# Kernel optimization log

Hardware: AMD Instinct MI355X
Metric: run time of the kernel (lower is better)

Reference implementation:

```python
import jax, jax.numpy as jnp
import numpy as np

NUM_HEADS = 16

def setup_inputs() -> dict:
    key = jax.random.key(0)
    k1, k2, k3 = jax.random.split(key, 3)
    B, S, D = 2, 2048, 1024
    return {
        "hidden_states": jax.random.normal(k1, (B, S, D), dtype=jnp.float32),
        "W_attn": jax.random.normal(k2, (D, 3 * D), dtype=jnp.float32) * 0.02,
        "b_attn": jnp.zeros((3 * D,), dtype=jnp.float32),
        "W_proj": jax.random.normal(k3, (D, D), dtype=jnp.float32) * 0.02,
        "b_proj": jnp.zeros((D,), dtype=jnp.float32),
    }

def reference(hidden_states, W_attn, b_attn, W_proj, b_proj):
    B, S, D = hidden_states.shape
    H = NUM_HEADS
    hd = D // H
    # qkv projection (Conv1D == addmm): [B,S,3D]
    qkv = hidden_states @ W_attn + b_attn
    q, k, v = jnp.split(qkv, 3, axis=-1)
    # split heads -> [B,H,S,hd]
    def split_heads(t):
        return t.reshape(B, S, H, hd).transpose(0, 2, 1, 3)
    q, k, v = split_heads(q), split_heads(k), split_heads(v)
    # scaled QK^T: [B,H,S,S]
    scores = jnp.einsum('bhqd,bhkd->bhqk', q, k) / jnp.asarray(hd ** 0.5, dtype=q.dtype)
    causal = jnp.tril(jnp.ones((S, S), dtype=bool))
    mask_value = jnp.finfo(scores.dtype).min
    scores = jnp.where(causal, scores, mask_value)
    probs = jax.nn.softmax(scores, axis=-1)  # attn_pdrop=0 -> no dropout
    out = jnp.einsum('bhqk,bhkd->bhqd', probs, v)
    # merge heads -> [B,S,D]
    out = out.transpose(0, 2, 1, 3).reshape(B, S, D)
    out = out @ W_proj + b_proj  # resid_pdrop=0 -> no dropout
    return out
```

## Files before the change

kernel.cpp:

```cpp
#include <hip/hip_runtime.h>
#include <math.h>

typedef __attribute__((ext_vector_type(8))) short bf16x8;
typedef __attribute__((ext_vector_type(4))) short bf16x4;
typedef __attribute__((ext_vector_type(4))) float f32x4;

#define MFMA16(a, b, c) __builtin_amdgcn_mfma_f32_16x16x32_bf16(a, b, c, 0, 0, 0)

#define GLOAD_LDS16(g, l)                                                        \
    __builtin_amdgcn_global_load_lds(                                            \
        (const __attribute__((address_space(1))) void*)(g),                      \
        (__attribute__((address_space(3))) void*)(l), 16, 0, 0)

__device__ __forceinline__ short f2bf(float f) {
    union { float f; unsigned u; } x; x.f = f;
    unsigned r = (x.u + 0x7fffu + ((x.u >> 16) & 1u)) >> 16;
    return (short)r;
}

__global__ __launch_bounds__(256) void convert_bf16_kernel(
    const float* __restrict__ in, short* __restrict__ out, int n4) {
    int i = blockIdx.x * 256 + threadIdx.x;
    if (i >= n4) return;
    float4 v = ((const float4*)in)[i];
    bf16x4 o;
    o[0] = f2bf(v.x); o[1] = f2bf(v.y); o[2] = f2bf(v.z); o[3] = f2bf(v.w);
    ((bf16x4*)out)[i] = o;
}

__global__ __launch_bounds__(256) void transpose_w2_kernel(
    const float* __restrict__ Wa, const float* __restrict__ Wp,
    short* __restrict__ WaT, short* __restrict__ WpT) {
    __shared__ float tile[32][33];
    const float* W; short* Wt; int N, xb;
    if (blockIdx.x < 96) { W = Wa; Wt = WaT; N = 3072; xb = blockIdx.x; }
    else                 { W = Wp; Wt = WpT; N = 1024; xb = blockIdx.x - 96; }
    const int K = 1024;
    int c = threadIdx.x & 31, r0 = threadIdx.x >> 5;
    int n0 = xb << 5, k0 = blockIdx.y << 5;
#pragma unroll
    for (int i = 0; i < 4; i++) {
        int r = r0 + i * 8;
        tile[r][c] = W[(long)(k0 + r) * N + n0 + c];
    }
    __syncthreads();
#pragma unroll
    for (int i = 0; i < 4; i++) {
        int r = r0 + i * 8;
        Wt[(long)(n0 + r) * K + k0 + c] = f2bf(tile[c][r]);
    }
}


#define SBAR() __builtin_amdgcn_s_barrier()
#define PRIO(x) __builtin_amdgcn_s_setprio(x)
#define VMW4 asm volatile("s_waitcnt vmcnt(4)" ::: "memory")
#define VMW2 asm volatile("s_waitcnt vmcnt(2)" ::: "memory")
#define VMW0 asm volatile("s_waitcnt vmcnt(0)" ::: "memory")
#define NOPS ((void)0)

#define LDA8(IDX) (*(const bf16x8*)&ls[(IDX)])
#define SA(q, k1v, nbv) GLOAD_LDS16(Ags + (size_t)(q) * 65536 + (k1v), &ls[(nbv) + (q) * 4096 + swd])
#define SB(q, k1v, nbv) GLOAD_LDS16(Bgs + (size_t)(q) * 65536 + (k1v), &ls[(nbv) + 32768 + (q) * 4096 + swd])

#define PHASE_MFMA(M0_, M1_, aa0, ba0, aa1, ba1)              \
    PRIO(1);                                                  \
    acc[M0_][0] = MFMA16(aa0, b00, acc[M0_][0]);              \
    acc[M0_][1] = MFMA16(aa0, b10, acc[M0_][1]);              \
    acc[M0_][2] = MFMA16(aa0, b20, acc[M0_][2]);              \
    acc[M0_][3] = MFMA16(aa0, b30, acc[M0_][3]);              \
    acc[M1_][0] = MFMA16(ba0, b00, acc[M1_][0]);              \
    acc[M1_][1] = MFMA16(ba0, b10, acc[M1_][1]);              \
    acc[M1_][2] = MFMA16(ba0, b20, acc[M1_][2]);              \
    acc[M1_][3] = MFMA16(ba0, b30, acc[M1_][3]);              \
    acc[M0_][0] = MFMA16(aa1, b01, acc[M0_][0]);              \
    acc[M0_][1] = MFMA16(aa1, b11, acc[M0_][1]);              \
    acc[M0_][2] = MFMA16(aa1, b21, acc[M0_][2]);              \
    acc[M0_][3] = MFMA16(aa1, b31, acc[M0_][3]);              \
    acc[M1_][0] = MFMA16(ba1, b01, acc[M1_][0]);              \
    acc[M1_][1] = MFMA16(ba1, b11, acc[M1_][1]);              \
    acc[M1_][2] = MFMA16(ba1, b21, acc[M1_][2]);              \
    acc[M1_][3] = MFMA16(ba1, b31, acc[M1_][3]);              \
    PRIO(0);

#define KTILE(T, STG, VMP2, VMTAIL) do {                                              \
    const int cb = ((T) & 1) << 14;                                                   \
    const int nb = cb ^ 16384;                                                        \
    const int k1 = ((T) + 1) << 6;                                                    \
    (void)nb; (void)k1;                                                               \
                                                                    \
    if (STG) { SB(0, k1, nb); SB(1, k1, nb); }                                        \
    const bf16x8 b00 = LDA8(cb + 32768 + bro + sw0);                                  \
    const bf16x8 b01 = LDA8(cb + 32768 + bro + sw1);                                  \
    const bf16x8 b10 = LDA8(cb + 32768 + bro + 1024 + sw0);                           \
    const bf16x8 b11 = LDA8(cb + 32768 + bro + 1024 + sw1);                           \
    const bf16x8 b20 = LDA8(cb + 32768 + bro + 2048 + sw0);                           \
    const bf16x8 b21 = LDA8(cb + 32768 + bro + 2048 + sw1);                           \
    const bf16x8 b30 = LDA8(cb + 32768 + bro + 3072 + sw0);                           \
    const bf16x8 b31 = LDA8(cb + 32768 + bro + 3072 + sw1);                           \
    {                                                                                 \
        bf16x8 x0 = LDA8(cb + aro + sw0), x1 = LDA8(cb + aro + sw1);                  \
        bf16x8 y0 = LDA8(cb + aro + 1024 + sw0), y1 = LDA8(cb + aro + 1024 + sw1);    \
        SBAR();                                                                       \
        PHASE_MFMA(0, 1, x0, y0, x1, y1)                                              \
        SBAR();                                                                       \
    }                                                                                 \
                                                                    \
    if (STG) { SB(2, k1, nb); SB(3, k1, nb); }                                        \
    {                                                                                 \
        bf16x8 x0 = LDA8(cb + aro + 2048 + sw0), x1 = LDA8(cb + aro + 2048 + sw1);    \
        bf16x8 y0 = LDA8(cb + aro + 3072 + sw0), y1 = LDA8(cb + aro + 3072 + sw1);    \
        SBAR();                                                                       \
        PHASE_MFMA(2, 3, x0, y0, x1, y1)                                              \
        SBAR();                                                                       \
    }                                                                                 \
                                                                    \
    VMP2;                                                                             \
    SBAR();                                                                           \
    if (STG) { SA(0, k1, nb); SA(2, k1, nb); }                                        \
    {                                                                                 \
        bf16x8 x0 = LDA8(cb + aro + 4096 + sw0), x1 = LDA8(cb + aro + 4096 + sw1);    \
        bf16x8 y0 = LDA8(cb + aro + 5120 + sw0), y1 = LDA8(cb + aro + 5120 + sw1);    \
        PHASE_MFMA(4, 5, x0, y0, x1, y1)                                              \
        SBAR();                                                                       \
    }                                                                                 \
                                                                    \
    if (STG) { SA(1, k1, nb); SA(3, k1, nb); }                                        \
    {                                                                                 \
        bf16x8 x0 = LDA8(cb + aro + 6144 + sw0), x1 = LDA8(cb + aro + 6144 + sw1);    \
        bf16x8 y0 = LDA8(cb + aro + 7168 + sw0), y1 = LDA8(cb + aro + 7168 + sw1);    \
        SBAR();                                                                       \
        PHASE_MFMA(6, 7, x0, y0, x1, y1)                                              \
        VMTAIL;                                                                       \
        SBAR();                                                                       \
    }                                                                                 \
} while (0)

__global__ __launch_bounds__(512, 2) void gemm_qkv_kernel(
    const short* __restrict__ A, const short* __restrict__ Bt,
    const float* __restrict__ bias,
    short* __restrict__ QK, short* __restrict__ VTb) {
    __shared__ __align__(16) short ls[65536];
    const int tid = threadIdx.x;
    const int lane = tid & 63, l15 = lane & 15, quad = lane >> 4;
    const int w = tid >> 6, wm = w >> 2, wn = w & 3;
    const int m0 = blockIdx.y * 256, n0 = blockIdx.x * 256;
    const int e = l15 & 7;
    const int sgr = (w << 3) + (lane >> 3);
    const int sgc = ((lane & 7) ^ (lane >> 3)) << 3;
    const int swd = w << 9;
    const short* Ags = A + (size_t)(m0 + sgr) * 1024 + sgc;
    const short* Bgs = Bt + (size_t)(n0 + sgr) * 1024 + sgc;
    const int aro = (wm * 128 + l15) << 6;
    const int bro = (wn * 64 + l15) << 6;
    const int sw0 = (quad ^ e) << 3;
    const int sw1 = ((4 + quad) ^ e) << 3;

    f32x4 acc[8][4];
#pragma unroll
    for (int i = 0; i < 8; i++)
#pragma unroll
        for (int j = 0; j < 4; j++) acc[i][j] = (f32x4){0.f, 0.f, 0.f, 0.f};

    SB(0, 0, 0); SB(1, 0, 0); SB(2, 0, 0); SB(3, 0, 0);
    SA(0, 0, 0); SA(2, 0, 0); SA(1, 0, 0); SA(3, 0, 0);
    VMW2;
    SBAR();

#pragma unroll 2
    for (int t = 0; t < 14; ++t) { KTILE(t, 1, VMW4, VMW2); }
    KTILE(14, 1, VMW4, VMW0);
    KTILE(15, 0, VMW0, NOPS);

    __syncthreads();

    if (n0 < 2048) {
        const float scale = (n0 < 1024) ? 0.18033688011112042f : 1.0f;
#pragma unroll
        for (int nt = 0; nt < 4; nt++) {
            const int nn = n0 + wn * 64 + nt * 16 + l15;
            const float bv = bias[nn];
#pragma unroll
            for (int mt = 0; mt < 8; mt++)
#pragma unroll
                for (int r = 0; r < 4; r++) {
                    const int mm = m0 + wm * 128 + mt * 16 + quad * 4 + r;
                    QK[(long)mm * 2048 + nn] = f2bf((acc[mt][nt][r] + bv) * scale);
                }
        }
    } else {
        short* vt = &ls[w * 4352];
        const int hh = ((n0 - 2048) >> 6) + wn;
        const int bb = m0 >> 11;
        const int srow = (m0 & 2047) + wm * 128;
        const int sloc = (lane & 7) << 3;
#pragma unroll
        for (int half = 0; half < 2; half++) {
#pragma unroll
            for (int nt = 0; nt < 4; nt++) {
                const int nn = n0 + wn * 64 + nt * 16 + l15;
                const float bv = bias[nn];
                const int d_ = nt * 16 + l15;
#pragma unroll
                for (int mt = 0; mt < 4; mt++) {
                    const int mtg = half * 4 + mt;
                    bf16x4 pk;
#pragma unroll
                    for (int r = 0; r < 4; r++) pk[r] = f2bf(acc[mtg][nt][r] + bv);
                    *(bf16x4*)&vt[d_ * 68 + mt * 16 + quad * 4] = pk;
                }
            }
#pragma unroll
            for (int i = 0; i < 8; i++) {
                const int d = i * 8 + (lane >> 3);
                bf16x8 vv = *(const bf16x8*)&vt[d * 68 + sloc];
                *(bf16x8*)&VTb[((size_t)(bb * 16 + hh) * 64 + d) * 2048 + srow + half * 64 + sloc] = vv;
            }
        }
    }
}

__global__ __launch_bounds__(256) void gemm_proj_kernel(
    const short* __restrict__ A, const short* __restrict__ Bt,
    const float* __restrict__ bias, float* __restrict__ outF) {
    __shared__ __align__(16) short lsA[128 * 64];
    __shared__ __align__(16) short lsB[64 * 64];
    const int tid = threadIdx.x;
    const int lane = tid & 63, l15 = lane & 15, quad = lane >> 4, w = tid >> 6;
    const int m0 = blockIdx.y * 128, n0 = blockIdx.x * 64;
    const int e = l15 & 7;
    const int lrow = lane >> 3;
    const int lgcol = ((lane & 7) ^ lrow) << 3;

    f32x4 acc[2][4];
#pragma unroll
    for (int i = 0; i < 2; i++)
#pragma unroll
        for (int j = 0; j < 4; j++) acc[i][j] = (f32x4){0.f, 0.f, 0.f, 0.f};

    for (int k0 = 0; k0 < 1024; k0 += 64) {
#pragma unroll
        for (int ii = 0; ii < 4; ii++) {
            const int i = (w << 2) + ii;
            const int grow = (i << 3) + lrow;
            GLOAD_LDS16(&A[(size_t)(m0 + grow) * 1024 + k0 + lgcol], &lsA[i * 512]);
        }
#pragma unroll
        for (int ii = 0; ii < 2; ii++) {
            const int i = (w << 1) + ii;
            const int grow = (i << 3) + lrow;
            GLOAD_LDS16(&Bt[(size_t)(n0 + grow) * 1024 + k0 + lgcol], &lsB[i * 512]);
        }
        __syncthreads();
#pragma unroll
        for (int kk = 0; kk < 64; kk += 32) {
            const int kb = kk >> 3;
            const int sw = (((kb + quad) ^ e) << 3);
            bf16x8 af[2], bfr[4];
#pragma unroll
            for (int mt = 0; mt < 2; mt++)
                af[mt] = *(const bf16x8*)&lsA[(w * 32 + mt * 16 + l15) * 64 + sw];
#pragma unroll
            for (int nt = 0; nt < 4; nt++)
                bfr[nt] = *(const bf16x8*)&lsB[(nt * 16 + l15) * 64 + sw];
#pragma unroll
            for (int mt = 0; mt < 2; mt++)
#pragma unroll
                for (int nt = 0; nt < 4; nt++)
                    acc[mt][nt] = MFMA16(af[mt], bfr[nt], acc[mt][nt]);
        }
        __syncthreads();
    }

#pragma unroll
    for (int nt = 0; nt < 4; nt++) {
        int nn = n0 + nt * 16 + l15;
        float bv = bias[nn];
#pragma unroll
        for (int mt = 0; mt < 2; mt++)
#pragma unroll
            for (int r = 0; r < 4; r++) {
                int mm = m0 + w * 32 + mt * 16 + quad * 4 + r;
                outF[(long)mm * 1024 + nn] = acc[mt][nt][r] + bv;
            }
    }
}

__global__ __launch_bounds__(256, 4) void attn_kernel(
    const short* __restrict__ QK, const short* __restrict__ VT,
    short* __restrict__ Ao) {
    __shared__ __align__(16) short Kt[2][64 * 64];
    __shared__ __align__(16) short Vt[2][64 * 64];
    __shared__ __align__(16) short Pt[4][1024];
    const int tid = threadIdx.x;
    const int lane = tid & 63, l15 = lane & 15, quad = lane >> 4, w = tid >> 6;
    const int bx = blockIdx.x;
    const int qt = 31 - (bx >> 5);
    const int hb = bx & 31;
    const int b = hb >> 4, h = hb & 15;
    const size_t rowbase = (size_t)b * 2048 * 2048 + h * 64;
    const short* Qb = QK + rowbase;
    const short* Kb = QK + rowbase + 1024;
    const short* Vh = VT + (size_t)hb * 64 * 2048;
    short* Pw = &Pt[w][0];
    const int e = l15 & 7;

    const int srow0 = tid >> 3, sc40 = (tid & 7) ^ (srow0 & 7);
    const int srow1 = srow0 + 32, sc41 = (tid & 7) ^ (srow1 & 7);
    const int sdst0 = srow0 * 64 + ((tid & 7) << 3);
    const int sdst1 = srow1 * 64 + ((tid & 7) << 3);

    const long qr = (long)(qt * 64 + w * 16 + l15) * 2048;
    bf16x8 qf0 = *(const bf16x8*)&Qb[qr + quad * 8];
    bf16x8 qf1 = *(const bf16x8*)&Qb[qr + 32 + quad * 8];

    float l = 0.f;
    f32x4 o[4];
#pragma unroll
    for (int dt = 0; dt < 4; dt++) o[dt] = (f32x4){0.f, 0.f, 0.f, 0.f};

    const int nc = qt + 1;

    *(bf16x8*)&Kt[0][sdst0] = *(const bf16x8*)&Kb[(size_t)srow0 * 2048 + sc40 * 8];
    *(bf16x8*)&Kt[0][sdst1] = *(const bf16x8*)&Kb[(size_t)srow1 * 2048 + sc41 * 8];
    *(bf16x8*)&Vt[0][sdst0] = *(const bf16x8*)&Vh[srow0 * 2048 + sc40 * 8];
    *(bf16x8*)&Vt[0][sdst1] = *(const bf16x8*)&Vh[srow1 * 2048 + sc41 * 8];
    __syncthreads();

    for (int c = 0; c < nc; c++) {
        const short* Kc = &Kt[c & 1][0];
        const short* Vc = &Vt[c & 1][0];
        const bool more = (c + 1 < nc);
        bf16x8 kr0, kr1, vr0, vr1;
        if (more) {
            const int k2 = (c + 1) * 64;
            kr0 = *(const bf16x8*)&Kb[(size_t)(k2 + srow0) * 2048 + sc40 * 8];
            kr1 = *(const bf16x8*)&Kb[(size_t)(k2 + srow1) * 2048 + sc41 * 8];
            vr0 = *(const bf16x8*)&Vh[srow0 * 2048 + k2 + sc40 * 8];
            vr1 = *(const bf16x8*)&Vh[srow1 * 2048 + k2 + sc41 * 8];
        }

        f32x4 s[4];
#pragma unroll
        for (int t = 0; t < 4; t++) {
            bf16x8 k0f = *(const bf16x8*)&Kc[(t * 16 + l15) * 64 + ((quad ^ e) << 3)];
            bf16x8 k1f = *(const bf16x8*)&Kc[(t * 16 + l15) * 64 + (((4 + quad) ^ e) << 3)];
            f32x4 z = (f32x4){0.f, 0.f, 0.f, 0.f};
            z = MFMA16(k0f, qf0, z);
            z = MFMA16(k1f, qf1, z);
            s[t] = z;
        }

        if (c == nc - 1) {
#pragma unroll
            for (int t = 0; t < 4; t++)
#pragma unroll
                for (int r = 0; r < 4; r++)
                    if (t * 16 + quad * 4 + r > w * 16 + l15) s[t][r] = -INFINITY;
        }

#pragma unroll
        for (int t = 0; t < 4; t++) {
            bf16x4 pw;
#pragma unroll
            for (int r = 0; r < 4; r++) {
                float pv = __builtin_amdgcn_exp2f(s[t][r]);
                l += pv;
                pw[r] = f2bf(pv);
            }
            *(bf16x4*)&Pw[l15 * 64 + (((2 * t + (quad >> 1)) ^ e) << 3) + ((quad & 1) << 2)] = pw;
        }

        bf16x8 pf0 = *(const bf16x8*)&Pw[l15 * 64 + ((quad ^ e) << 3)];
        bf16x8 pf1 = *(const bf16x8*)&Pw[l15 * 64 + (((4 + quad) ^ e) << 3)];
#pragma unroll
        for (int dt = 0; dt < 4; dt++) {
            bf16x8 v0f = *(const bf16x8*)&Vc[(dt * 16 + l15) * 64 + ((quad ^ e) << 3)];
            bf16x8 v1f = *(const bf16x8*)&Vc[(dt * 16 + l15) * 64 + (((4 + quad) ^ e) << 3)];
            o[dt] = MFMA16(v0f, pf0, o[dt]);
            o[dt] = MFMA16(v1f, pf1, o[dt]);
        }

        if (more) {
            short* Kn = &Kt[(c + 1) & 1][0];
            short* Vn = &Vt[(c + 1) & 1][0];
            *(bf16x8*)&Kn[sdst0] = kr0;
            *(bf16x8*)&Kn[sdst1] = kr1;
            *(bf16x8*)&Vn[sdst0] = vr0;
            *(bf16x8*)&Vn[sdst1] = vr1;
        }
        __syncthreads();
    }

    l += __shfl_xor(l, 16);
    l += __shfl_xor(l, 32);
    const float rl = 1.f / l;

    const int qs = qt * 64 + w * 16 + l15;
    const long base = ((long)(b * 2048 + qs)) * 1024 + h * 64;
#pragma unroll
    for (int dt = 0; dt < 4; dt++) {
        bf16x4 wv;
#pragma unroll
        for (int r = 0; r < 4; r++) wv[r] = f2bf(o[dt][r] * rl);
        *(bf16x4*)&Ao[base + dt * 16 + quad * 4] = wv;
    }
}

extern "C" void kernel_launch(void* const* d_in, const int* in_sizes, int n_in,
                              void* d_out, int out_size, void* d_ws, size_t ws_size,
                              hipStream_t stream) {
    const float* hs = (const float*)d_in[0];
    const float* W_attn = (const float*)d_in[1];
    const float* b_attn = (const float*)d_in[2];
    const float* W_proj = (const float*)d_in[3];
    const float* b_proj = (const float*)d_in[4];
    float* out = (float*)d_out;

    const size_t MB = 1024 * 1024;
    char* ws = (char*)d_ws;
    short* hs_bf = (short*)ws;
    short* attn_o = hs_bf;
    short* WaT = (short*)(ws + 8 * MB);
    short* WpT = (short*)(ws + 14 * MB);
    short* QK = (short*)(ws + 16 * MB);
    short* VTb = (short*)(ws + 32 * MB);

    convert_bf16_kernel<<<4096, 256, 0, stream>>>(hs, hs_bf, 1048576);
    transpose_w2_kernel<<<dim3(128, 32), 256, 0, stream>>>(W_attn, W_proj, WaT, WpT);
    gemm_qkv_kernel<<<dim3(12, 16), 512, 0, stream>>>(hs_bf, WaT, b_attn, QK, VTb);
    attn_kernel<<<1024, 256, 0, stream>>>(QK, VTb, attn_o);
    gemm_proj_kernel<<<dim3(16, 32), 256, 0, stream>>>(attn_o, WpT, b_proj, out);
}
```

Before: 167.9 us.

## Merge prep kernels, triple-buffer proj GEMM, pair causal q-tiles in attention

Fuses the hidden-state bf16 conversion and the weight transpose into one prep launch, saving a kernel launch. The projection GEMM now uses a triple-buffered LDS pipeline with vmcnt waits and raw barriers instead of two syncthreads per k-step. The attention kernel gives each block a long and a short query tile (qt and 31-qt) to balance causal work, halving the grid, and raises MFMA priority around its matmuls. The trade-offs are more LDS per proj block and fewer, longer attention blocks, which lowers parallelism.

```diff
diff --git a/kernel.cpp b/kernel.cpp
--- a/kernel.cpp
+++ b/kernel.cpp
@@ -12,32 +12,43 @@
         (const __attribute__((address_space(1))) void*)(g),                      \
         (__attribute__((address_space(3))) void*)(l), 16, 0, 0)
 
+#define SBAR() __builtin_amdgcn_s_barrier()
+#define PRIO(x) __builtin_amdgcn_s_setprio(x)
+#define VMW6 asm volatile("s_waitcnt vmcnt(6)" ::: "memory")
+#define VMW4 asm volatile("s_waitcnt vmcnt(4)" ::: "memory")
+#define VMW2 asm volatile("s_waitcnt vmcnt(2)" ::: "memory")
+#define VMW0 asm volatile("s_waitcnt vmcnt(0)" ::: "memory")
+#define NOPS ((void)0)
+
 __device__ __forceinline__ short f2bf(float f) {
     union { float f; unsigned u; } x; x.f = f;
     unsigned r = (x.u + 0x7fffu + ((x.u >> 16) & 1u)) >> 16;
     return (short)r;
 }
 
-__global__ __launch_bounds__(256) void convert_bf16_kernel(
-    const float* __restrict__ in, short* __restrict__ out, int n4) {
-    int i = blockIdx.x * 256 + threadIdx.x;
-    if (i >= n4) return;
-    float4 v = ((const float4*)in)[i];
-    bf16x4 o;
-    o[0] = f2bf(v.x); o[1] = f2bf(v.y); o[2] = f2bf(v.z); o[3] = f2bf(v.w);
-    ((bf16x4*)out)[i] = o;
-}
-
-__global__ __launch_bounds__(256) void transpose_w2_kernel(
+__global__ __launch_bounds__(256) void prep_kernel(
+    const float* __restrict__ hs, short* __restrict__ hs_bf,
     const float* __restrict__ Wa, const float* __restrict__ Wp,
     short* __restrict__ WaT, short* __restrict__ WpT) {
     __shared__ float tile[32][33];
+    const int bid = blockIdx.x;
+    if (bid < 4096) {
+        int i = bid * 256 + threadIdx.x;
+        float4 v = ((const float4*)hs)[i];
+        bf16x4 o;
+        o[0] = f2bf(v.x); o[1] = f2bf(v.y); o[2] = f2bf(v.z); o[3] = f2bf(v.w);
+        ((bf16x4*)hs_bf)[i] = o;
+        return;
+    }
+    const int xb2 = bid - 4096;
+    const int xbb = xb2 & 127;
+    const int ky = xb2 >> 7;
     const float* W; short* Wt; int N, xb;
-    if (blockIdx.x < 96) { W = Wa; Wt = WaT; N = 3072; xb = blockIdx.x; }
-    else                 { W = Wp; Wt = WpT; N = 1024; xb = blockIdx.x - 96; }
+    if (xbb < 96) { W = Wa; Wt = WaT; N = 3072; xb = xbb; }
+    else          { W = Wp; Wt = WpT; N = 1024; xb = xbb - 96; }
     const int K = 1024;
     int c = threadIdx.x & 31, r0 = threadIdx.x >> 5;
-    int n0 = xb << 5, k0 = blockIdx.y << 5;
+    int n0 = xb << 5, k0 = ky << 5;
 #pragma unroll
     for (int i = 0; i < 4; i++) {
         int r = r0 + i * 8;
@@ -50,14 +61,6 @@
         Wt[(long)(n0 + r) * K + k0 + c] = f2bf(tile[c][r]);
     }
 }
-
-
-#define SBAR() __builtin_amdgcn_s_barrier()
-#define PRIO(x) __builtin_amdgcn_s_setprio(x)
-#define VMW4 asm volatile("s_waitcnt vmcnt(4)" ::: "memory")
-#define VMW2 asm volatile("s_waitcnt vmcnt(2)" ::: "memory")
-#define VMW0 asm volatile("s_waitcnt vmcnt(0)" ::: "memory")
-#define NOPS ((void)0)
 
 #define LDA8(IDX) (*(const bf16x8*)&ls[(IDX)])
 #define SA(q, k1v, nbv) GLOAD_LDS16(Ags + (size_t)(q) * 65536 + (k1v), &ls[(nbv) + (q) * 4096 + swd])
@@ -220,17 +223,29 @@
     }
 }
 
-__global__ __launch_bounds__(256) void gemm_proj_kernel(
+#define PJ_ISSUE(K0, BB) do {                                                               \
+    const int i0 = (w << 2);                                                                \
+    GLOAD_LDS16(&Ap[(size_t)((i0 << 3) + lrow) * 1024 + (K0) + lgcol], &ls[(BB) + i0 * 512]);             \
+    GLOAD_LDS16(&Ap[(size_t)(((i0 + 1) << 3) + lrow) * 1024 + (K0) + lgcol], &ls[(BB) + (i0 + 1) * 512]); \
+    GLOAD_LDS16(&Ap[(size_t)(((i0 + 2) << 3) + lrow) * 1024 + (K0) + lgcol], &ls[(BB) + (i0 + 2) * 512]); \
+    GLOAD_LDS16(&Ap[(size_t)(((i0 + 3) << 3) + lrow) * 1024 + (K0) + lgcol], &ls[(BB) + (i0 + 3) * 512]); \
+    const int j0 = (w << 1);                                                                \
+    GLOAD_LDS16(&Bp[(size_t)((j0 << 3) + lrow) * 1024 + (K0) + lgcol], &ls[(BB) + 8192 + j0 * 512]);      \
+    GLOAD_LDS16(&Bp[(size_t)(((j0 + 1) << 3) + lrow) * 1024 + (K0) + lgcol], &ls[(BB) + 8192 + (j0 + 1) * 512]); \
+} while (0)
+
+__global__ __launch_bounds__(256, 2) void gemm_proj_kernel(
     const short* __restrict__ A, const short* __restrict__ Bt,
     const float* __restrict__ bias, float* __restrict__ outF) {
-    __shared__ __align__(16) short lsA[128 * 64];
-    __shared__ __align__(16) short lsB[64 * 64];
+    __shared__ __align__(16) short ls[36864];
     const int tid = threadIdx.x;
     const int lane = tid & 63, l15 = lane & 15, quad = lane >> 4, w = tid >> 6;
     const int m0 = blockIdx.y * 128, n0 = blockIdx.x * 64;
     const int e = l15 & 7;
     const int lrow = lane >> 3;
     const int lgcol = ((lane & 7) ^ lrow) << 3;
+    const short* Ap = A + (size_t)m0 * 1024;
+    const short* Bp = Bt + (size_t)n0 * 1024;
 
     f32x4 acc[2][4];
 #pragma unroll
@@ -238,38 +253,41 @@
 #pragma unroll
         for (int j = 0; j < 4; j++) acc[i][j] = (f32x4){0.f, 0.f, 0.f, 0.f};
 
-    for (int k0 = 0; k0 < 1024; k0 += 64) {
-#pragma unroll
-        for (int ii = 0; ii < 4; ii++) {
-            const int i = (w << 2) + ii;
-            const int grow = (i << 3) + lrow;
-            GLOAD_LDS16(&A[(size_t)(m0 + grow) * 1024 + k0 + lgcol], &lsA[i * 512]);
-        }
-#pragma unroll
-        for (int ii = 0; ii < 2; ii++) {
-            const int i = (w << 1) + ii;
-            const int grow = (i << 3) + lrow;
-            GLOAD_LDS16(&Bt[(size_t)(n0 + grow) * 1024 + k0 + lgcol], &lsB[i * 512]);
-        }
-        __syncthreads();
-#pragma unroll
-        for (int kk = 0; kk < 64; kk += 32) {
-            const int kb = kk >> 3;
+    PJ_ISSUE(0, 0);
+    PJ_ISSUE(64, 12288);
+    VMW6;
+    SBAR();
+
+    int cur = 0;
+    for (int t = 0; t < 16; ++t) {
+        const int bb = cur * 12288;
+        if (t < 14) {
+            const int nb2 = (cur == 0) ? 24576 : (cur - 1) * 12288;
+            PJ_ISSUE((t + 2) << 6, nb2);
+        }
+#pragma unroll
+        for (int kb = 0; kb < 8; kb += 4) {
             const int sw = (((kb + quad) ^ e) << 3);
-            bf16x8 af[2], bfr[4];
-#pragma unroll
-            for (int mt = 0; mt < 2; mt++)
-                af[mt] = *(const bf16x8*)&lsA[(w * 32 + mt * 16 + l15) * 64 + sw];
-#pragma unroll
-            for (int nt = 0; nt < 4; nt++)
-                bfr[nt] = *(const bf16x8*)&lsB[(nt * 16 + l15) * 64 + sw];
-#pragma unroll
-            for (int mt = 0; mt < 2; mt++)
-#pragma unroll
-                for (int nt = 0; nt < 4; nt++)
-                    acc[mt][nt] = MFMA16(af[mt], bfr[nt], acc[mt][nt]);
-        }
-        __syncthreads();
+            bf16x8 af0 = *(const bf16x8*)&ls[bb + (w * 32 + l15) * 64 + sw];
+            bf16x8 af1 = *(const bf16x8*)&ls[bb + (w * 32 + 16 + l15) * 64 + sw];
+            bf16x8 bf0 = *(const bf16x8*)&ls[bb + 8192 + (l15) * 64 + sw];
+            bf16x8 bf1 = *(const bf16x8*)&ls[bb + 8192 + (16 + l15) * 64 + sw];
+            bf16x8 bf2 = *(const bf16x8*)&ls[bb + 8192 + (32 + l15) * 64 + sw];
+            bf16x8 bf3 = *(const bf16x8*)&ls[bb + 8192 + (48 + l15) * 64 + sw];
+            PRIO(1);
+            acc[0][0] = MFMA16(af0, bf0, acc[0][0]);
+            acc[0][1] = MFMA16(af0, bf1, acc[0][1]);
+            acc[0][2] = MFMA16(af0, bf2, acc[0][2]);
+            acc[0][3] = MFMA16(af0, bf3, acc[0][3]);
+            acc[1][0] = MFMA16(af1, bf0, acc[1][0]);
+            acc[1][1] = MFMA16(af1, bf1, acc[1][1]);
+            acc[1][2] = MFMA16(af1, bf2, acc[1][2]);
+            acc[1][3] = MFMA16(af1, bf3, acc[1][3]);
+            PRIO(0);
+        }
+        if (t < 14) { VMW6; SBAR(); }
+        else if (t == 14) { VMW0; SBAR(); }
+        cur = (cur == 2) ? 0 : cur + 1;
     }
 
 #pragma unroll
@@ -295,7 +313,7 @@
     const int tid = threadIdx.x;
     const int lane = tid & 63, l15 = lane & 15, quad = lane >> 4, w = tid >> 6;
     const int bx = blockIdx.x;
-    const int qt = 31 - (bx >> 5);
+    const int p = bx >> 5;
     const int hb = bx & 31;
     const int b = hb >> 4, h = hb & 15;
     const size_t rowbase = (size_t)b * 2048 * 2048 + h * 64;
@@ -310,100 +328,107 @@
     const int sdst0 = srow0 * 64 + ((tid & 7) << 3);
     const int sdst1 = srow1 * 64 + ((tid & 7) << 3);
 
-    const long qr = (long)(qt * 64 + w * 16 + l15) * 2048;
-    bf16x8 qf0 = *(const bf16x8*)&Qb[qr + quad * 8];
-    bf16x8 qf1 = *(const bf16x8*)&Qb[qr + 32 + quad * 8];
-
-    float l = 0.f;
-    f32x4 o[4];
-#pragma unroll
-    for (int dt = 0; dt < 4; dt++) o[dt] = (f32x4){0.f, 0.f, 0.f, 0.f};
-
-    const int nc = qt + 1;
-
-    *(bf16x8*)&Kt[0][sdst0] = *(const bf16x8*)&Kb[(size_t)srow0 * 2048 + sc40 * 8];
-    *(bf16x8*)&Kt[0][sdst1] = *(const bf16x8*)&Kb[(size_t)srow1 * 2048 + sc41 * 8];
-    *(bf16x8*)&Vt[0][sdst0] = *(const bf16x8*)&Vh[srow0 * 2048 + sc40 * 8];
-    *(bf16x8*)&Vt[0][sdst1] = *(const bf16x8*)&Vh[srow1 * 2048 + sc41 * 8];
-    __syncthreads();
-
-    for (int c = 0; c < nc; c++) {
-        const short* Kc = &Kt[c & 1][0];
-        const short* Vc = &Vt[c & 1][0];
-        const bool more = (c + 1 < nc);
-        bf16x8 kr0, kr1, vr0, vr1;
-        if (more) {
-            const int k2 = (c + 1) * 64;
-            kr0 = *(const bf16x8*)&Kb[(size_t)(k2 + srow0) * 2048 + sc40 * 8];
-            kr1 = *(const bf16x8*)&Kb[(size_t)(k2 + srow1) * 2048 + sc41 * 8];
-            vr0 = *(const bf16x8*)&Vh[srow0 * 2048 + k2 + sc40 * 8];
-            vr1 = *(const bf16x8*)&Vh[srow1 * 2048 + k2 + sc41 * 8];
-        }
-
-        f32x4 s[4];
-#pragma unroll
-        for (int t = 0; t < 4; t++) {
-            bf16x8 k0f = *(const bf16x8*)&Kc[(t * 16 + l15) * 64 + ((quad ^ e) << 3)];
-            bf16x8 k1f = *(const bf16x8*)&Kc[(t * 16 + l15) * 64 + (((4 + quad) ^ e) << 3)];
-            f32x4 z = (f32x4){0.f, 0.f, 0.f, 0.f};
-            z = MFMA16(k0f, qf0, z);
-            z = MFMA16(k1f, qf1, z);
-            s[t] = z;
-        }
-
-        if (c == nc - 1) {
-#pragma unroll
-            for (int t = 0; t < 4; t++)
-#pragma unroll
-                for (int r = 0; r < 4; r++)
-                    if (t * 16 + quad * 4 + r > w * 16 + l15) s[t][r] = -INFINITY;
-        }
-
-#pragma unroll
-        for (int t = 0; t < 4; t++) {
-            bf16x4 pw;
-#pragma unroll
-            for (int r = 0; r < 4; r++) {
-                float pv = __builtin_amdgcn_exp2f(s[t][r]);
-                l += pv;
-                pw[r] = f2bf(pv);
-            }
-            *(bf16x4*)&Pw[l15 * 64 + (((2 * t + (quad >> 1)) ^ e) << 3) + ((quad & 1) << 2)] = pw;
-        }
-
-        bf16x8 pf0 = *(const bf16x8*)&Pw[l15 * 64 + ((quad ^ e) << 3)];
-        bf16x8 pf1 = *(const bf16x8*)&Pw[l15 * 64 + (((4 + quad) ^ e) << 3)];
+    for (int half = 0; half < 2; half++) {
+        const int qt = half ? p : (31 - p);
+        const int nc = qt + 1;
+
+        const long qr = (long)(qt * 64 + w * 16 + l15) * 2048;
+        bf16x8 qf0 = *(const bf16x8*)&Qb[qr + quad * 8];
+        bf16x8 qf1 = *(const bf16x8*)&Qb[qr + 32 + quad * 8];
+
+        float l = 0.f;
+        f32x4 o[4];
+#pragma unroll
+        for (int dt = 0; dt < 4; dt++) o[dt] = (f32x4){0.f, 0.f, 0.f, 0.f};
+
+        *(bf16x8*)&Kt[0][sdst0] = *(const bf16x8*)&Kb[(size_t)srow0 * 2048 + sc40 * 8];
+        *(bf16x8*)&Kt[0][sdst1] = *(const bf16x8*)&Kb[(size_t)srow1 * 2048 + sc41 * 8];
+        *(bf16x8*)&Vt[0][sdst0] = *(const bf16x8*)&Vh[srow0 * 2048 + sc40 * 8];
+        *(bf16x8*)&Vt[0][sdst1] = *(const bf16x8*)&Vh[srow1 * 2048 + sc41 * 8];
+        __syncthreads();
+
+        for (int c = 0; c < nc; c++) {
+            const short* Kc = &Kt[c & 1][0];
+            const short* Vc = &Vt[c & 1][0];
+            const bool more = (c + 1 < nc);
+            bf16x8 kr0, kr1, vr0, vr1;
+            if (more) {
+                const int k2 = (c + 1) * 64;
+                kr0 = *(const bf16x8*)&Kb[(size_t)(k2 + srow0) * 2048 + sc40 * 8];
+                kr1 = *(const bf16x8*)&Kb[(size_t)(k2 + srow1) * 2048 + sc41 * 8];
+                vr0 = *(const bf16x8*)&Vh[srow0 * 2048 + k2 + sc40 * 8];
+                vr1 = *(const bf16x8*)&Vh[srow1 * 2048 + k2 + sc41 * 8];
+            }
+
+            f32x4 s[4];
+            PRIO(1);
+#pragma unroll
+            for (int t = 0; t < 4; t++) {
+                bf16x8 k0f = *(const bf16x8*)&Kc[(t * 16 + l15) * 64 + ((quad ^ e) << 3)];
+                bf16x8 k1f = *(const bf16x8*)&Kc[(t * 16 + l15) * 64 + (((4 + quad) ^ e) << 3)];
+                f32x4 z = (f32x4){0.f, 0.f, 0.f, 0.f};
+                z = MFMA16(k0f, qf0, z);
+                z = MFMA16(k1f, qf1, z);
+                s[t] = z;
+            }
+            PRIO(0);
+
+            if (c == nc - 1) {
+#pragma unroll
+                for (int t = 0; t < 4; t++)
+#pragma unroll
+                    for (int r = 0; r < 4; r++)
+                        if (t * 16 + quad * 4 + r > w * 16 + l15) s[t][r] = -INFINITY;
+            }
+
+#pragma unroll
+            for (int t = 0; t < 4; t++) {
+                bf16x4 pw;
+#pragma unroll
+                for (int r = 0; r < 4; r++) {
+                    float pv = __builtin_amdgcn_exp2f(s[t][r]);
+                    l += pv;
+                    pw[r] = f2bf(pv);
+                }
+                *(bf16x4*)&Pw[l15 * 64 + (((2 * t + (quad >> 1)) ^ e) << 3) + ((quad & 1) << 2)] = pw;
+            }
+
+            bf16x8 pf0 = *(const bf16x8*)&Pw[l15 * 64 + ((quad ^ e) << 3)];
+            bf16x8 pf1 = *(const bf16x8*)&Pw[l15 * 64 + (((4 + quad) ^ e) << 3)];
+            PRIO(1);
+#pragma unroll
+            for (int dt = 0; dt < 4; dt++) {
+                bf16x8 v0f = *(const bf16x8*)&Vc[(dt * 16 + l15) * 64 + ((quad ^ e) << 3)];
+                bf16x8 v1f = *(const bf16x8*)&Vc[(dt * 16 + l15) * 64 + (((4 + quad) ^ e) << 3)];
+                o[dt] = MFMA16(v0f, pf0, o[dt]);
+                o[dt] = MFMA16(v1f, pf1, o[dt]);
+            }
+            PRIO(0);
+
+            if (more) {
+                short* Kn = &Kt[(c + 1) & 1][0];
+                short* Vn = &Vt[(c + 1) & 1][0];
+                *(bf16x8*)&Kn[sdst0] = kr0;
+                *(bf16x8*)&Kn[sdst1] = kr1;
+                *(bf16x8*)&Vn[sdst0] = vr0;
+                *(bf16x8*)&Vn[sdst1] = vr1;
+            }
+            __syncthreads();
+        }
+
+        l += __shfl_xor(l, 16);
+        l += __shfl_xor(l, 32);
+        const float rl = 1.f / l;
+
+        const int qs = qt * 64 + w * 16 + l15;
+        const long base = ((long)(b * 2048 + qs)) * 1024 + h * 64;
 #pragma unroll
         for (int dt = 0; dt < 4; dt++) {
-            bf16x8 v0f = *(const bf16x8*)&Vc[(dt * 16 + l15) * 64 + ((quad ^ e) << 3)];
-            bf16x8 v1f = *(const bf16x8*)&Vc[(dt * 16 + l15) * 64 + (((4 + quad) ^ e) << 3)];
-            o[dt] = MFMA16(v0f, pf0, o[dt]);
-            o[dt] = MFMA16(v1f, pf1, o[dt]);
-        }
-
-        if (more) {
-            short* Kn = &Kt[(c + 1) & 1][0];
-            short* Vn = &Vt[(c + 1) & 1][0];
-            *(bf16x8*)&Kn[sdst0] = kr0;
-            *(bf16x8*)&Kn[sdst1] = kr1;
-            *(bf16x8*)&Vn[sdst0] = vr0;
-            *(bf16x8*)&Vn[sdst1] = vr1;
-        }
-        __syncthreads();
-    }
-
-    l += __shfl_xor(l, 16);
-    l += __shfl_xor(l, 32);
-    const float rl = 1.f / l;
-
-    const int qs = qt * 64 + w * 16 + l15;
-    const long base = ((long)(b * 2048 + qs)) * 1024 + h * 64;
-#pragma unroll
-    for (int dt = 0; dt < 4; dt++) {
-        bf16x4 wv;
-#pragma unroll
-        for (int r = 0; r < 4; r++) wv[r] = f2bf(o[dt][r] * rl);
-        *(bf16x4*)&Ao[base + dt * 16 + quad * 4] = wv;
+            bf16x4 wv;
+#pragma unroll
+            for (int r = 0; r < 4; r++) wv[r] = f2bf(o[dt][r] * rl);
+            *(bf16x4*)&Ao[base + dt * 16 + quad * 4] = wv;
+        }
     }
 }
 
@@ -426,9 +451,8 @@
     short* QK = (short*)(ws + 16 * MB);
     short* VTb = (short*)(ws + 32 * MB);
 
-    convert_bf16_kernel<<<4096, 256, 0, stream>>>(hs, hs_bf, 1048576);
-    transpose_w2_kernel<<<dim3(128, 32), 256, 0, stream>>>(W_attn, W_proj, WaT, WpT);
+    prep_kernel<<<8192, 256, 0, stream>>>(hs, hs_bf, W_attn, W_proj, WaT, WpT);
     gemm_qkv_kernel<<<dim3(12, 16), 512, 0, stream>>>(hs_bf, WaT, b_attn, QK, VTb);
-    attn_kernel<<<1024, 256, 0, stream>>>(QK, VTb, attn_o);
+    attn_kernel<<<512, 256, 0, stream>>>(QK, VTb, attn_o);
     gemm_proj_kernel<<<dim3(16, 32), 256, 0, stream>>>(attn_o, WpT, b_proj, out);
 }
```

Measured after the change: 172.5 us. 1.03x slower.
